# Kernel tuning notes

Hardware: AMD Instinct MI355X
Metric: run time of the kernel (lower is better)

Reference implementation:

```python
import jax, jax.numpy as jnp
import numpy as np

N = 768      # n_proto (number of class prototypes)
D = 128      # trans_feat_num
H = D // 16  # edge-MLP hidden = 8
A = 312      # semantic attribute dim
INIT_TEMP = 0.1
VTEMP = 10.0
STEMP = 10.0
EPS = 1e-8


def _layer_norm(x, g, b, eps=1e-5):
    m = x.mean(-1, keepdims=True)
    v = ((x - m) ** 2).mean(-1, keepdims=True)
    return (x - m) / jnp.sqrt(v + eps) * g + b


def _instance_norm_rows(x, eps=1e-5):
    # torch InstanceNorm1d on 2D input: unbatched (C, L) -> normalize each row, no affine
    m = x.mean(-1, keepdims=True)
    v = ((x - m) ** 2).mean(-1, keepdims=True)
    return (x - m) / jnp.sqrt(v + eps)


def _init_edge(x, temp):
    # pairwise cosine similarity + row softmax
    nrm = jnp.linalg.norm(x, axis=1)
    sim = (x @ x.T) / jnp.maximum(nrm[:, None] * nrm[None, :], EPS)
    return jax.nn.softmax(sim / temp, axis=-1)


def _edge_update(proto, last_edge, W1, b1, W2, b2, temp):
    n, d = proto.shape
    # O(n^2) pairwise squared differences  -> [n*n, d]
    feat = ((proto[:, None, :] - proto[None, :, :]) ** 2).reshape(n * n, d)
    h = jax.nn.relu(_instance_norm_rows(feat @ W1.T + b1))  # [n*n, H]
    e = jnp.tanh(h @ W2.T + b2).reshape(n, n)
    return jax.nn.softmax(e * (last_edge + EPS) / temp, axis=-1)


def _node_update(proto, last_edge, edge, W, b, g, beta):
    extra = last_edge @ proto          # cross-modal message (dist_injection)
    p = edge @ proto                   # same-modal aggregation
    return jax.nn.relu(_layer_norm((p + extra) @ W.T + b, g, beta)) + p


def setup_inputs() -> dict:
    key = jax.random.key(0)
    ks = jax.random.split(key, 9)
    rn = lambda k, shape, s=1.0: jax.random.normal(k, shape, dtype=jnp.float32) * s
    return {
        "visual_proto": rn(ks[0], (N, D)),
        "semantic_proto": rn(ks[1], (N, D)),
        "attribute": rn(ks[2], (N, A)),
        "Wvn": rn(ks[3], (D, D), 0.08), "bvn": jnp.zeros((D,), jnp.float32),
        "gvn": jnp.ones((D,), jnp.float32), "betavn": jnp.zeros((D,), jnp.float32),
        "Wve1": rn(ks[4], (H, D), 0.1), "bve1": jnp.zeros((H,), jnp.float32),
        "Wve2": rn(ks[5], (1, H), 0.3), "bve2": jnp.zeros((1,), jnp.float32),
        "Wsn": rn(ks[6], (D, D), 0.08), "bsn": jnp.zeros((D,), jnp.float32),
        "gsn": jnp.ones((D,), jnp.float32), "betasn": jnp.zeros((D,), jnp.float32),
        "Wse1": rn(ks[7], (H, D), 0.1), "bse1": jnp.zeros((H,), jnp.float32),
        "Wse2": rn(ks[8], (1, H), 0.3), "bse2": jnp.zeros((1,), jnp.float32),
    }


def reference(visual_proto, semantic_proto, attribute,
              Wvn, bvn, gvn, betavn, Wve1, bve1, Wve2, bve2,
              Wsn, bsn, gsn, betasn, Wse1, bse1, Wse2, bse2):
    ve = _init_edge(visual_proto, INIT_TEMP)
    se = _init_edge(attribute, INIT_TEMP)
    vp = _node_update(visual_proto, se, ve, Wvn, bvn, gvn, betavn)
    ve2 = _edge_update(vp, ve, Wve1, bve1, Wve2, bve2, VTEMP)
    sp = _node_update(semantic_proto, ve2, se, Wsn, bsn, gsn, betasn)
    se2 = _edge_update(sp, se, Wse1, bse1, Wse2, bse2, STEMP)
    return vp, sp, ve2, se2
```

## Files before the change

kernel.cpp:

```cpp
#include <hip/hip_runtime.h>
#include <math.h>

#define NN 768
#define DD 128
#define AA 312
#define HH 8
#define CEPS 1e-8f

typedef __attribute__((ext_vector_type(8))) short s8b;
typedef __attribute__((ext_vector_type(4))) float f4v;

__device__ __forceinline__ float wave_sum(float v) {
    #pragma unroll
    for (int o = 32; o; o >>= 1) v += __shfl_down(v, o, 64);
    return v;
}
__device__ __forceinline__ float wave_max(float v) {
    #pragma unroll
    for (int o = 32; o; o >>= 1) v = fmaxf(v, __shfl_down(v, o, 64));
    return v;
}
__device__ __forceinline__ unsigned short f2bf(float f) {
    unsigned u = __float_as_uint(f);
    u += 0x7FFFu + ((u >> 16) & 1u);
    return (unsigned short)(u >> 16);
}

template <int COLS>
__device__ void gram_tile(const float* __restrict__ A, float invtemp, float* __restrict__ sim,
                          int i0, int j0, int tid, float* As, float* Bs) {
    const int tx = tid & 15, ty = tid >> 4;
    const int lr = tid >> 3, lc4 = (tid & 7) * 4;
    float acc00 = 0.f, acc01 = 0.f, acc10 = 0.f, acc11 = 0.f;
    float si0 = 0.f, si1 = 0.f, sj0 = 0.f, sj1 = 0.f;
    for (int kc = 0; kc < COLS; kc += 32) {
        float4 av, bv;
        if (kc + lc4 + 4 <= COLS) {
            av = *(const float4*)(A + (size_t)(i0 + lr) * COLS + kc + lc4);
            bv = *(const float4*)(A + (size_t)(j0 + lr) * COLS + kc + lc4);
        } else {
            float ta[4], tb[4];
            #pragma unroll
            for (int l = 0; l < 4; ++l) {
                int c = kc + lc4 + l;
                ta[l] = (c < COLS) ? A[(size_t)(i0 + lr) * COLS + c] : 0.f;
                tb[l] = (c < COLS) ? A[(size_t)(j0 + lr) * COLS + c] : 0.f;
            }
            av = make_float4(ta[0], ta[1], ta[2], ta[3]);
            bv = make_float4(tb[0], tb[1], tb[2], tb[3]);
        }
        __syncthreads();
        As[(lc4 + 0) * 34 + lr] = av.x; As[(lc4 + 1) * 34 + lr] = av.y;
        As[(lc4 + 2) * 34 + lr] = av.z; As[(lc4 + 3) * 34 + lr] = av.w;
        Bs[(lc4 + 0) * 34 + lr] = bv.x; Bs[(lc4 + 1) * 34 + lr] = bv.y;
        Bs[(lc4 + 2) * 34 + lr] = bv.z; Bs[(lc4 + 3) * 34 + lr] = bv.w;
        __syncthreads();
        #pragma unroll
        for (int k = 0; k < 32; ++k) {
            float2 aa = *(const float2*)&As[k * 34 + 2 * ty];
            float2 bb = *(const float2*)&Bs[k * 34 + 2 * tx];
            acc00 = fmaf(aa.x, bb.x, acc00);
            acc01 = fmaf(aa.x, bb.y, acc01);
            acc10 = fmaf(aa.y, bb.x, acc10);
            acc11 = fmaf(aa.y, bb.y, acc11);
            si0 = fmaf(aa.x, aa.x, si0);
            si1 = fmaf(aa.y, aa.y, si1);
            sj0 = fmaf(bb.x, bb.x, sj0);
            sj1 = fmaf(bb.y, bb.y, sj1);
        }
    }
    const float ni0 = sqrtf(si0), ni1 = sqrtf(si1);
    const float nj0 = sqrtf(sj0), nj1 = sqrtf(sj1);
    float* s0 = sim + (size_t)(i0 + 2 * ty) * NN + j0 + 2 * tx;
    float* s1 = s0 + NN;
    s0[0] = acc00 / fmaxf(ni0 * nj0, CEPS) * invtemp;
    s0[1] = acc01 / fmaxf(ni0 * nj1, CEPS) * invtemp;
    s1[0] = acc10 / fmaxf(ni1 * nj0, CEPS) * invtemp;
    s1[1] = acc11 / fmaxf(ni1 * nj1, CEPS) * invtemp;
}

__global__ __launch_bounds__(256) void gram_prep_kernel(
    const float* __restrict__ visual, const float* __restrict__ attribute,
    const float* __restrict__ Wvn, const float* __restrict__ Wsn, float* __restrict__ simv,
    float* __restrict__ sima, float* __restrict__ WvnT, float* __restrict__ WsnT) {
    __shared__ __align__(16) float smem[2176];
    const int tid = threadIdx.x;
    const int task = blockIdx.x;
    if (task < 576) {
        gram_tile<DD>(visual, 10.f, simv, (task / 24) * 32, (task % 24) * 32, tid, smem,
                      smem + 1088);
    } else if (task < 1152) {
        const int rem = task - 576;
        gram_tile<AA>(attribute, 10.f, sima, (rem / 24) * 32, (rem % 24) * 32, tid, smem,
                      smem + 1088);
    } else {
        const int u = task - 1152;
        const float* S = (u >= 16) ? Wsn : Wvn;
        float* Dt = (u >= 16) ? WsnT : WvnT;
        const int tile = u & 15;
        const int c0 = (tile & 3) * 32, r0 = (tile >> 2) * 32;
        const int tx = tid & 31, ty = tid >> 5;
        #pragma unroll
        for (int rr = ty; rr < 32; rr += 8)
            smem[rr * 33 + tx] = S[(size_t)(r0 + rr) * DD + c0 + tx];
        __syncthreads();
        #pragma unroll
        for (int rr = ty; rr < 32; rr += 8)
            Dt[(size_t)(c0 + rr) * DD + r0 + tx] = smem[tx * 33 + rr];
    }
}

__device__ void softmax_row_g(const float* __restrict__ vr, float* __restrict__ dst, int tid,
                              float* red) {
    float v0 = vr[tid], v1 = vr[tid + 256], v2 = vr[tid + 512];
    float m = wave_max(fmaxf(fmaxf(v0, v1), v2));
    if ((tid & 63) == 0) red[tid >> 6] = m;
    __syncthreads();
    m = fmaxf(fmaxf(red[0], red[1]), fmaxf(red[2], red[3]));
    float e0 = __expf(v0 - m), e1 = __expf(v1 - m), e2 = __expf(v2 - m);
    float sw = wave_sum(e0 + e1 + e2);
    if ((tid & 63) == 0) red[4 + (tid >> 6)] = sw;
    __syncthreads();
    const float s = red[4] + red[5] + red[6] + red[7];
    const float inv = 1.f / s;
    dst[tid] = e0 * inv;
    dst[tid + 256] = e1 * inv;
    dst[tid + 512] = e2 * inv;
}

__global__ __launch_bounds__(256) void softmax_all_kernel(const float* __restrict__ simv,
                                                          const float* __restrict__ sima,
                                                          float* __restrict__ ve,
                                                          float* __restrict__ se) {
    __shared__ float red[8];
    const int task = blockIdx.x;
    const float* src = (task < NN) ? simv + (size_t)task * NN : sima + (size_t)(task - NN) * NN;
    float* dst = (task < NN) ? ve + (size_t)task * NN : se + (size_t)(task - NN) * NN;
    softmax_row_g(src, dst, threadIdx.x, red);
}

__global__ __launch_bounds__(256) void softmax_out_kernel(const float* __restrict__ L,
                                                          float* __restrict__ dst) {
    __shared__ float red[8];
    const int i = blockIdx.x;
    softmax_row_g(L + (size_t)i * NN, dst + (size_t)i * NN, threadIdx.x, red);
}

__device__ void block_softmax768(float* buf, int tid, float* red) {
    const int w = tid >> 6, lane = tid & 63;
    float v0 = buf[tid];
    float v1 = (tid < NN - 512) ? buf[tid + 512] : -3.4e38f;
    float m = wave_max(fmaxf(v0, v1));
    if (lane == 0) red[w] = m;
    __syncthreads();
    m = red[0];
    #pragma unroll
    for (int i = 1; i < 8; ++i) m = fmaxf(m, red[i]);
    float e0 = __expf(v0 - m);
    float e1 = (tid < NN - 512) ? __expf(v1 - m) : 0.f;
    float sw = wave_sum(e0 + e1);
    if (lane == 0) red[8 + w] = sw;
    __syncthreads();
    float s = 0.f;
    #pragma unroll
    for (int i = 0; i < 8; ++i) s += red[8 + i];
    const float inv = 1.f / s;
    buf[tid] = e0 * inv;
    if (tid < NN - 512) buf[tid + 512] = e1 * inv;
    __syncthreads();
}

template <bool EXSM>
__global__ __launch_bounds__(512) void node_kernel(
    const float* __restrict__ P, const float* __restrict__ Ep, const float* __restrict__ ExOrL,
    const float* __restrict__ WT, const float* __restrict__ b, const float* __restrict__ g,
    const float* __restrict__ beta, float* __restrict__ out, const float* __restrict__ W1e,
    short* __restrict__ outb, float* __restrict__ cvec, float* __restrict__ exOut) {
    __shared__ __align__(16) float ep[2][NN], ex[2][NN];
    __shared__ __align__(16) float pp[4][2][DD], xx[4][2][DD];
    __shared__ __align__(16) float qs[2][DD], tps[2][2][DD];
    __shared__ float red[16];
    const int i0 = blockIdx.x * 2;
    const int tid = threadIdx.x;
    const int s = (tid >> 7) & 3, d = tid & 127;
    #pragma unroll
    for (int r = 0; r < 2; ++r)
        for (int k = tid; k < NN; k += 512) {
            ep[r][k] = Ep[(size_t)(i0 + r) * NN + k];
            ex[r][k] = ExOrL[(size_t)(i0 + r) * NN + k];
        }
    __syncthreads();
    if (EXSM) {
        block_softmax768(ex[0], tid, red);
        block_softmax768(ex[1], tid, red);
        #pragma unroll
        for (int r = 0; r < 2; ++r)
            for (int k = tid; k < NN; k += 512) exOut[(size_t)(i0 + r) * NN + k] = ex[r][k];
    }
    float p0 = 0.f, x0 = 0.f, p1 = 0.f, x1 = 0.f;
    const int kb = s * 192;
    #pragma unroll 4
    for (int kk = 0; kk < 192; ++kk) {
        const int k = kb + kk;
        const float pv = P[(size_t)k * DD + d];
        p0 = fmaf(ep[0][k], pv, p0);
        x0 = fmaf(ex[0][k], pv, x0);
        p1 = fmaf(ep[1][k], pv, p1);
        x1 = fmaf(ex[1][k], pv, x1);
    }
    pp[s][0][d] = p0; xx[s][0][d] = x0;
    pp[s][1][d] = p1; xx[s][1][d] = x1;
    __syncthreads();
    const int rr = (tid >> 7) & 1;
    float preg = 0.f;
    if (tid < 256) {
        float p = pp[0][rr][d] + pp[1][rr][d] + pp[2][rr][d] + pp[3][rr][d];
        float x = xx[0][rr][d] + xx[1][rr][d] + xx[2][rr][d] + xx[3][rr][d];
        qs[rr][d] = p + x;
        preg = p;
    }
    __syncthreads();
    {
        const int sc = tid >> 8, rr2 = (tid >> 7) & 1;
        float t = (sc == 0) ? b[d] : 0.f;
        const int c0 = sc * 64;
        #pragma unroll 4
        for (int c = c0; c < c0 + 64; ++c) t = fmaf(qs[rr2][c], WT[(size_t)c * DD + d], t);
        tps[sc][rr2][d] = t;
    }
    __syncthreads();
    float tval = 0.f;
    if (tid < 256) tval = tps[0][rr][d] + tps[1][rr][d];
    float sm = wave_sum(tid < 256 ? tval : 0.f);
    if ((tid & 63) == 0) red[tid >> 6] = sm;
    __syncthreads();
    if (tid < 256) tval -= (red[2 * rr] + red[2 * rr + 1]) * (1.f / DD);
    float s2 = wave_sum(tid < 256 ? tval * tval : 0.f);
    if ((tid & 63) == 0) red[8 + (tid >> 6)] = s2;
    __syncthreads();
    if (tid < 256) {
        const float var = (red[8 + 2 * rr] + red[8 + 2 * rr + 1]) * (1.f / DD);
        const float ln = tval * rsqrtf(var + 1e-5f) * g[d] + beta[d];
        const float val = fmaxf(ln, 0.f) + preg;
        out[(size_t)(i0 + rr) * DD + d] = val;
        outb[(size_t)(i0 + rr) * DD + d] = (short)f2bf(val);
        qs[rr][d] = val;
    }
    __syncthreads();
    if (tid < 16) {
        const int row = tid >> 3, r = tid & 7;
        float ssum = 0.f;
        for (int k = 0; k < DD; ++k) {
            const float pv = qs[row][k];
            ssum = fmaf(W1e[r * DD + k], pv * pv, ssum);
        }
        cvec[(size_t)(i0 + row) * HH + r] = ssum;
    }
}

__global__ __launch_bounds__(256) void edge_gemm_kernel(
    const float* __restrict__ PR, const short* __restrict__ PRb, const float* __restrict__ cvec,
    const float* __restrict__ Elast, const float* __restrict__ W1, const float* __restrict__ b1,
    const float* __restrict__ W2, const float* __restrict__ b2, float invtemp,
    float* __restrict__ Lout) {
    const int bp = blockIdx.x / 3;
    const int i0 = bp * 2;
    const int jbase = (blockIdx.x % 3) * 256;
    const int tid = threadIdx.x;
    const int lane = tid & 63, wave = tid >> 6;
    __shared__ __align__(16) float pi[2][DD];
    __shared__ __align__(16) float w1s[HH * DD];
    __shared__ __align__(16) short a_sw[4 * 64 * 8];
    if (tid < 256) pi[tid >> 7][tid & 127] = PR[(size_t)(i0 + (tid >> 7)) * DD + (tid & 127)];
    ((float4*)w1s)[tid] = ((const float4*)W1)[tid];
    __syncthreads();
    {
        const int t = tid >> 6, m = lane & 15, q = lane >> 4;
        const int il = m >> 3, r = m & 7;
        const int kb = t * 32 + q * 8;
        s8b av;
        #pragma unroll
        for (int e = 0; e < 8; ++e)
            av[e] = (short)f2bf(pi[il][kb + e] * w1s[r * DD + kb + e]);
        *(s8b*)&a_sw[(t * 64 + lane) * 8] = av;
    }
    __syncthreads();
    s8b af[4];
    #pragma unroll
    for (int t = 0; t < 4; ++t) af[t] = *(const s8b*)&a_sw[(t * 64 + lane) * 8];
    const int q = lane >> 4, n = lane & 15;
    const int rbase = (q & 1) * 4;
    const int il = q >> 1;
    const float4 ci4 = *(const float4*)&cvec[(size_t)(i0 + il) * HH + rbase];
    const float4 b14 = *(const float4*)&b1[rbase];
    const float4 w24 = *(const float4*)&W2[rbase];
    const float b2s = b2[0];
    #pragma unroll
    for (int s = 0; s < 4; ++s) {
        const int j = jbase + (wave * 4 + s) * 16 + n;
        f4v acc = {0.f, 0.f, 0.f, 0.f};
        #pragma unroll
        for (int t = 0; t < 4; ++t) {
            const s8b bf = *(const s8b*)(PRb + (size_t)j * DD + t * 32 + q * 8);
            acc = __builtin_amdgcn_mfma_f32_16x16x32_bf16(af[t], bf, acc, 0, 0, 0);
        }
        const float4 cj = *(const float4*)&cvec[(size_t)j * HH + rbase];
        float z[4];
        z[0] = ci4.x + cj.x - 2.f * acc[0] + b14.x;
        z[1] = ci4.y + cj.y - 2.f * acc[1] + b14.y;
        z[2] = ci4.z + cj.z - 2.f * acc[2] + b14.z;
        z[3] = ci4.w + cj.w - 2.f * acc[3] + b14.w;
        float s1 = z[0] + z[1] + z[2] + z[3];
        float s2 = z[0] * z[0] + z[1] * z[1] + z[2] * z[2] + z[3] * z[3];
        s1 += __shfl_xor(s1, 16, 64);
        s2 += __shfl_xor(s2, 16, 64);
        const float mean = s1 * (1.f / HH);
        const float var = fmaxf(s2 * (1.f / HH) - mean * mean, 0.f);
        const float istd = rsqrtf(var + 1e-5f);
        float a2 = 0.f;
        a2 = fmaf(fmaxf((z[0] - mean) * istd, 0.f), w24.x, a2);
        a2 = fmaf(fmaxf((z[1] - mean) * istd, 0.f), w24.y, a2);
        a2 = fmaf(fmaxf((z[2] - mean) * istd, 0.f), w24.z, a2);
        a2 = fmaf(fmaxf((z[3] - mean) * istd, 0.f), w24.w, a2);
        a2 += __shfl_xor(a2, 16, 64);
        const float tv = tanhf(a2 + b2s);
        const float lv = Elast[(size_t)(i0 + il) * NN + j];
        if ((q & 1) == 0) Lout[(size_t)(i0 + il) * NN + j] = tv * (lv + CEPS) * invtemp;
    }
}

extern "C" void kernel_launch(void* const* d_in, const int* in_sizes, int n_in, void* d_out,
                              int out_size, void* d_ws, size_t ws_size, hipStream_t stream) {
    const float* visual    = (const float*)d_in[0];
    const float* semantic  = (const float*)d_in[1];
    const float* attribute = (const float*)d_in[2];
    const float* Wvn  = (const float*)d_in[3];
    const float* bvn  = (const float*)d_in[4];
    const float* gvn  = (const float*)d_in[5];
    const float* betavn = (const float*)d_in[6];
    const float* Wve1 = (const float*)d_in[7];
    const float* bve1 = (const float*)d_in[8];
    const float* Wve2 = (const float*)d_in[9];
    const float* bve2 = (const float*)d_in[10];
    const float* Wsn  = (const float*)d_in[11];
    const float* bsn  = (const float*)d_in[12];
    const float* gsn  = (const float*)d_in[13];
    const float* betasn = (const float*)d_in[14];
    const float* Wse1 = (const float*)d_in[15];
    const float* bse1 = (const float*)d_in[16];
    const float* Wse2 = (const float*)d_in[17];
    const float* bse2 = (const float*)d_in[18];

    float* out = (float*)d_out;
    float* vp  = out;
    float* sp  = out + 98304;
    float* ve2 = out + 196608;
    float* se2 = out + 786432;

    float* ws    = (float*)d_ws;
    float* simv  = ws;
    float* sima  = ws + 589824;
    float* ve    = ws + 1179648;
    float* se    = ws + 1769472;
    float* L     = ws + 2359296;
    float* WvnT  = ws + 2949120;
    float* WsnT  = ws + 2965504;
    float* cvec1 = ws + 2981888;
    float* cvec2 = ws + 2988032;
    short* vpb   = (short*)(ws + 2994176);
    short* spb   = (short*)(ws + 3043328);

    gram_prep_kernel<<<1184, 256, 0, stream>>>(visual, attribute, Wvn, Wsn, simv, sima, WvnT,
                                               WsnT);
    softmax_all_kernel<<<1536, 256, 0, stream>>>(simv, sima, ve, se);
    node_kernel<false><<<NN / 2, 512, 0, stream>>>(visual, ve, se, WvnT, bvn, gvn, betavn, vp,
                                                   Wve1, vpb, cvec1, nullptr);
    edge_gemm_kernel<<<(NN / 2) * 3, 256, 0, stream>>>(vp, vpb, cvec1, ve, Wve1, bve1, Wve2,
                                                       bve2, 0.1f, L);
    node_kernel<true><<<NN / 2, 512, 0, stream>>>(semantic, se, L, WsnT, bsn, gsn, betasn, sp,
                                                  Wse1, spb, cvec2, ve2);
    edge_gemm_kernel<<<(NN / 2) * 3, 256, 0, stream>>>(sp, spb, cvec2, se, Wse1, bse1, Wse2,
                                                       bse2, 0.1f, L);
    softmax_out_kernel<<<NN, 256, 0, stream>>>(L, se2);
}
```

Measured before the change: 196.2 us.

## Fuse init-edge softmax and output softmax into node and edge kernels

The Gram kernel now writes raw dot products plus per-row inverse norms taken from the diagonal tiles. Cosine scaling and the row softmax are recomputed inside the node and edge kernels, so the separate softmax launches and the ve/se/L round trips through global memory go away. The edge kernel now handles full rows, 384 blocks of 512 threads, and applies the final softmax in shared memory before writing the output. In exchange, softmax work is repeated in several kernels, the edge kernel has fewer and larger blocks with more shared memory, and norms now come from the Gram diagonal instead of a separate sum of squares.

After: 203.5 us. 3.7% more time.

```diff
diff --git a/kernel.cpp b/kernel.cpp
--- a/kernel.cpp
+++ b/kernel.cpp
@@ -26,13 +26,37 @@
     return (unsigned short)(u >> 16);
 }
 
+__device__ void block_softmax768(float* buf, int tid, float* red) {
+    const int w = tid >> 6, lane = tid & 63;
+    float v0 = buf[tid];
+    float v1 = (tid < NN - 512) ? buf[tid + 512] : -3.4e38f;
+    float m = wave_max(fmaxf(v0, v1));
+    if (lane == 0) red[w] = m;
+    __syncthreads();
+    m = red[0];
+    #pragma unroll
+    for (int i = 1; i < 8; ++i) m = fmaxf(m, red[i]);
+    float e0 = __expf(v0 - m);
+    float e1 = (tid < NN - 512) ? __expf(v1 - m) : 0.f;
+    float sw = wave_sum(e0 + e1);
+    if (lane == 0) red[8 + w] = sw;
+    __syncthreads();
+    float s = 0.f;
+    #pragma unroll
+    for (int i = 0; i < 8; ++i) s += red[8 + i];
+    const float inv = 1.f / s;
+    buf[tid] = e0 * inv;
+    if (tid < NN - 512) buf[tid + 512] = e1 * inv;
+    __syncthreads();
+}
+
 template <int COLS>
-__device__ void gram_tile(const float* __restrict__ A, float invtemp, float* __restrict__ sim,
-                          int i0, int j0, int tid, float* As, float* Bs) {
+__device__ void gram_tile_raw(const float* __restrict__ A, float* __restrict__ sim,
+                              float* __restrict__ invn, int i0, int j0, int tid, float* As,
+                              float* Bs) {
     const int tx = tid & 15, ty = tid >> 4;
     const int lr = tid >> 3, lc4 = (tid & 7) * 4;
     float acc00 = 0.f, acc01 = 0.f, acc10 = 0.f, acc11 = 0.f;
-    float si0 = 0.f, si1 = 0.f, sj0 = 0.f, sj1 = 0.f;
     for (int kc = 0; kc < COLS; kc += 32) {
         float4 av, bv;
         if (kc + lc4 + 4 <= COLS) {
@@ -63,36 +87,33 @@
             acc01 = fmaf(aa.x, bb.y, acc01);
             acc10 = fmaf(aa.y, bb.x, acc10);
             acc11 = fmaf(aa.y, bb.y, acc11);
-            si0 = fmaf(aa.x, aa.x, si0);
-            si1 = fmaf(aa.y, aa.y, si1);
-            sj0 = fmaf(bb.x, bb.x, sj0);
-            sj1 = fmaf(bb.y, bb.y, sj1);
-        }
-    }
-    const float ni0 = sqrtf(si0), ni1 = sqrtf(si1);
-    const float nj0 = sqrtf(sj0), nj1 = sqrtf(sj1);
+        }
+    }
     float* s0 = sim + (size_t)(i0 + 2 * ty) * NN + j0 + 2 * tx;
     float* s1 = s0 + NN;
-    s0[0] = acc00 / fmaxf(ni0 * nj0, CEPS) * invtemp;
-    s0[1] = acc01 / fmaxf(ni0 * nj1, CEPS) * invtemp;
-    s1[0] = acc10 / fmaxf(ni1 * nj0, CEPS) * invtemp;
-    s1[1] = acc11 / fmaxf(ni1 * nj1, CEPS) * invtemp;
+    s0[0] = acc00; s0[1] = acc01;
+    s1[0] = acc10; s1[1] = acc11;
+    if (i0 == j0 && tx == ty) {
+        invn[i0 + 2 * tx] = 1.f / sqrtf(fmaxf(acc00, 1e-24f));
+        invn[i0 + 2 * tx + 1] = 1.f / sqrtf(fmaxf(acc11, 1e-24f));
+    }
 }
 
 __global__ __launch_bounds__(256) void gram_prep_kernel(
     const float* __restrict__ visual, const float* __restrict__ attribute,
     const float* __restrict__ Wvn, const float* __restrict__ Wsn, float* __restrict__ simv,
-    float* __restrict__ sima, float* __restrict__ WvnT, float* __restrict__ WsnT) {
+    float* __restrict__ sima, float* __restrict__ WvnT, float* __restrict__ WsnT,
+    float* __restrict__ invnv, float* __restrict__ invna) {
     __shared__ __align__(16) float smem[2176];
     const int tid = threadIdx.x;
     const int task = blockIdx.x;
     if (task < 576) {
-        gram_tile<DD>(visual, 10.f, simv, (task / 24) * 32, (task % 24) * 32, tid, smem,
-                      smem + 1088);
+        gram_tile_raw<DD>(visual, simv, invnv, (task / 24) * 32, (task % 24) * 32, tid, smem,
+                          smem + 1088);
     } else if (task < 1152) {
         const int rem = task - 576;
-        gram_tile<AA>(attribute, 10.f, sima, (rem / 24) * 32, (rem % 24) * 32, tid, smem,
-                      smem + 1088);
+        gram_tile_raw<AA>(attribute, sima, invna, (rem / 24) * 32, (rem % 24) * 32, tid, smem,
+                          smem + 1088);
     } else {
         const int u = task - 1152;
         const float* S = (u >= 16) ? Wsn : Wvn;
@@ -110,72 +131,13 @@
     }
 }
 
-__device__ void softmax_row_g(const float* __restrict__ vr, float* __restrict__ dst, int tid,
-                              float* red) {
-    float v0 = vr[tid], v1 = vr[tid + 256], v2 = vr[tid + 512];
-    float m = wave_max(fmaxf(fmaxf(v0, v1), v2));
-    if ((tid & 63) == 0) red[tid >> 6] = m;
-    __syncthreads();
-    m = fmaxf(fmaxf(red[0], red[1]), fmaxf(red[2], red[3]));
-    float e0 = __expf(v0 - m), e1 = __expf(v1 - m), e2 = __expf(v2 - m);
-    float sw = wave_sum(e0 + e1 + e2);
-    if ((tid & 63) == 0) red[4 + (tid >> 6)] = sw;
-    __syncthreads();
-    const float s = red[4] + red[5] + red[6] + red[7];
-    const float inv = 1.f / s;
-    dst[tid] = e0 * inv;
-    dst[tid + 256] = e1 * inv;
-    dst[tid + 512] = e2 * inv;
-}
-
-__global__ __launch_bounds__(256) void softmax_all_kernel(const float* __restrict__ simv,
-                                                          const float* __restrict__ sima,
-                                                          float* __restrict__ ve,
-                                                          float* __restrict__ se) {
-    __shared__ float red[8];
-    const int task = blockIdx.x;
-    const float* src = (task < NN) ? simv + (size_t)task * NN : sima + (size_t)(task - NN) * NN;
-    float* dst = (task < NN) ? ve + (size_t)task * NN : se + (size_t)(task - NN) * NN;
-    softmax_row_g(src, dst, threadIdx.x, red);
-}
-
-__global__ __launch_bounds__(256) void softmax_out_kernel(const float* __restrict__ L,
-                                                          float* __restrict__ dst) {
-    __shared__ float red[8];
-    const int i = blockIdx.x;
-    softmax_row_g(L + (size_t)i * NN, dst + (size_t)i * NN, threadIdx.x, red);
-}
-
-__device__ void block_softmax768(float* buf, int tid, float* red) {
-    const int w = tid >> 6, lane = tid & 63;
-    float v0 = buf[tid];
-    float v1 = (tid < NN - 512) ? buf[tid + 512] : -3.4e38f;
-    float m = wave_max(fmaxf(v0, v1));
-    if (lane == 0) red[w] = m;
-    __syncthreads();
-    m = red[0];
-    #pragma unroll
-    for (int i = 1; i < 8; ++i) m = fmaxf(m, red[i]);
-    float e0 = __expf(v0 - m);
-    float e1 = (tid < NN - 512) ? __expf(v1 - m) : 0.f;
-    float sw = wave_sum(e0 + e1);
-    if (lane == 0) red[8 + w] = sw;
-    __syncthreads();
-    float s = 0.f;
-    #pragma unroll
-    for (int i = 0; i < 8; ++i) s += red[8 + i];
-    const float inv = 1.f / s;
-    buf[tid] = e0 * inv;
-    if (tid < NN - 512) buf[tid + 512] = e1 * inv;
-    __syncthreads();
-}
-
 template <bool EXSM>
 __global__ __launch_bounds__(512) void node_kernel(
-    const float* __restrict__ P, const float* __restrict__ Ep, const float* __restrict__ ExOrL,
-    const float* __restrict__ WT, const float* __restrict__ b, const float* __restrict__ g,
-    const float* __restrict__ beta, float* __restrict__ out, const float* __restrict__ W1e,
-    short* __restrict__ outb, float* __restrict__ cvec, float* __restrict__ exOut) {
+    const float* __restrict__ P, const float* __restrict__ EpRaw,
+    const float* __restrict__ invnP, const float* __restrict__ Ex,
+    const float* __restrict__ invnX, const float* __restrict__ WT, const float* __restrict__ b,
+    const float* __restrict__ g, const float* __restrict__ beta, float* __restrict__ out,
+    const float* __restrict__ W1e, short* __restrict__ outb, float* __restrict__ cvec) {
     __shared__ __align__(16) float ep[2][NN], ex[2][NN];
     __shared__ __align__(16) float pp[4][2][DD], xx[4][2][DD];
     __shared__ __align__(16) float qs[2][DD], tps[2][2][DD];
@@ -183,19 +145,23 @@
     const int i0 = blockIdx.x * 2;
     const int tid = threadIdx.x;
     const int s = (tid >> 7) & 3, d = tid & 127;
+    const float cp0 = 10.f * invnP[i0], cp1 = 10.f * invnP[i0 + 1];
+    const float cx0 = EXSM ? 10.f * invnX[i0] : 0.f;
+    const float cx1 = EXSM ? 10.f * invnX[i0 + 1] : 0.f;
     #pragma unroll
     for (int r = 0; r < 2; ++r)
         for (int k = tid; k < NN; k += 512) {
-            ep[r][k] = Ep[(size_t)(i0 + r) * NN + k];
-            ex[r][k] = ExOrL[(size_t)(i0 + r) * NN + k];
-        }
-    __syncthreads();
+            ep[r][k] = EpRaw[(size_t)(i0 + r) * NN + k] * (r ? cp1 : cp0) * invnP[k];
+            float x = Ex[(size_t)(i0 + r) * NN + k];
+            if (EXSM) x *= (r ? cx1 : cx0) * invnX[k];
+            ex[r][k] = x;
+        }
+    __syncthreads();
+    block_softmax768(ep[0], tid, red);
+    block_softmax768(ep[1], tid, red);
     if (EXSM) {
         block_softmax768(ex[0], tid, red);
         block_softmax768(ex[1], tid, red);
-        #pragma unroll
-        for (int r = 0; r < 2; ++r)
-            for (int k = tid; k < NN; k += 512) exOut[(size_t)(i0 + r) * NN + k] = ex[r][k];
     }
     float p0 = 0.f, x0 = 0.f, p1 = 0.f, x1 = 0.f;
     const int kb = s * 192;
@@ -258,23 +224,31 @@
     }
 }
 
-__global__ __launch_bounds__(256) void edge_gemm_kernel(
+__global__ __launch_bounds__(512) void edge_full_kernel(
     const float* __restrict__ PR, const short* __restrict__ PRb, const float* __restrict__ cvec,
-    const float* __restrict__ Elast, const float* __restrict__ W1, const float* __restrict__ b1,
-    const float* __restrict__ W2, const float* __restrict__ b2, float invtemp,
-    float* __restrict__ Lout) {
-    const int bp = blockIdx.x / 3;
-    const int i0 = bp * 2;
-    const int jbase = (blockIdx.x % 3) * 256;
+    const float* __restrict__ lastRaw, const float* __restrict__ invnL,
+    const float* __restrict__ W1, const float* __restrict__ b1, const float* __restrict__ W2,
+    const float* __restrict__ b2, float invtemp, float* __restrict__ Eout) {
+    const int i0 = blockIdx.x * 2;
     const int tid = threadIdx.x;
     const int lane = tid & 63, wave = tid >> 6;
     __shared__ __align__(16) float pi[2][DD];
     __shared__ __align__(16) float w1s[HH * DD];
     __shared__ __align__(16) short a_sw[4 * 64 * 8];
+    __shared__ __align__(16) float lrow[2][NN];
+    __shared__ __align__(16) float logits[2][NN];
+    __shared__ float red[16];
     if (tid < 256) pi[tid >> 7][tid & 127] = PR[(size_t)(i0 + (tid >> 7)) * DD + (tid & 127)];
-    ((float4*)w1s)[tid] = ((const float4*)W1)[tid];
-    __syncthreads();
-    {
+    else ((float4*)w1s)[tid - 256] = ((const float4*)W1)[tid - 256];
+    const float cl0 = 10.f * invnL[i0], cl1 = 10.f * invnL[i0 + 1];
+    #pragma unroll
+    for (int r = 0; r < 2; ++r)
+        for (int k = tid; k < NN; k += 512)
+            lrow[r][k] = lastRaw[(size_t)(i0 + r) * NN + k] * (r ? cl1 : cl0) * invnL[k];
+    __syncthreads();
+    block_softmax768(lrow[0], tid, red);
+    block_softmax768(lrow[1], tid, red);
+    if (tid < 256) {
         const int t = tid >> 6, m = lane & 15, q = lane >> 4;
         const int il = m >> 3, r = m & 7;
         const int kb = t * 32 + q * 8;
@@ -296,8 +270,8 @@
     const float4 w24 = *(const float4*)&W2[rbase];
     const float b2s = b2[0];
     #pragma unroll
-    for (int s = 0; s < 4; ++s) {
-        const int j = jbase + (wave * 4 + s) * 16 + n;
+    for (int s = 0; s < 6; ++s) {
+        const int j = (wave * 6 + s) * 16 + n;
         f4v acc = {0.f, 0.f, 0.f, 0.f};
         #pragma unroll
         for (int t = 0; t < 4; ++t) {
@@ -324,9 +298,15 @@
         a2 = fmaf(fmaxf((z[3] - mean) * istd, 0.f), w24.w, a2);
         a2 += __shfl_xor(a2, 16, 64);
         const float tv = tanhf(a2 + b2s);
-        const float lv = Elast[(size_t)(i0 + il) * NN + j];
-        if ((q & 1) == 0) Lout[(size_t)(i0 + il) * NN + j] = tv * (lv + CEPS) * invtemp;
-    }
+        if ((q & 1) == 0) logits[il][j] = tv * (lrow[il][j] + CEPS) * invtemp;
+    }
+    __syncthreads();
+    block_softmax768(logits[0], tid, red);
+    block_softmax768(logits[1], tid, red);
+    #pragma unroll
+    for (int r = 0; r < 2; ++r)
+        for (int k = tid; k < NN; k += 512)
+            Eout[(size_t)(i0 + r) * NN + k] = logits[r][k];
 }
 
 extern "C" void kernel_launch(void* const* d_in, const int* in_sizes, int n_in, void* d_out,
@@ -360,26 +340,23 @@
     float* ws    = (float*)d_ws;
     float* simv  = ws;
     float* sima  = ws + 589824;
-    float* ve    = ws + 1179648;
-    float* se    = ws + 1769472;
-    float* L     = ws + 2359296;
-    float* WvnT  = ws + 2949120;
-    float* WsnT  = ws + 2965504;
-    float* cvec1 = ws + 2981888;
-    float* cvec2 = ws + 2988032;
-    short* vpb   = (short*)(ws + 2994176);
-    short* spb   = (short*)(ws + 3043328);
+    float* WvnT  = ws + 1179648;
+    float* WsnT  = ws + 1196032;
+    float* invnv = ws + 1212416;
+    float* invna = ws + 1213184;
+    float* cvec1 = ws + 1213952;
+    float* cvec2 = ws + 1220096;
+    short* vpb   = (short*)(ws + 1226240);
+    short* spb   = (short*)(ws + 1275392);
 
     gram_prep_kernel<<<1184, 256, 0, stream>>>(visual, attribute, Wvn, Wsn, simv, sima, WvnT,
-                                               WsnT);
-    softmax_all_kernel<<<1536, 256, 0, stream>>>(simv, sima, ve, se);
-    node_kernel<false><<<NN / 2, 512, 0, stream>>>(visual, ve, se, WvnT, bvn, gvn, betavn, vp,
-                                                   Wve1, vpb, cvec1, nullptr);
-    edge_gemm_kernel<<<(NN / 2) * 3, 256, 0, stream>>>(vp, vpb, cvec1, ve, Wve1, bve1, Wve2,
-                                                       bve2, 0.1f, L);
-    node_kernel<true><<<NN / 2, 512, 0, stream>>>(semantic, se, L, WsnT, bsn, gsn, betasn, sp,
-                                                  Wse1, spb, cvec2, ve2);
-    edge_gemm_kernel<<<(NN / 2) * 3, 256, 0, stream>>>(sp, spb, cvec2, se, Wse1, bse1, Wse2,
-                                                       bse2, 0.1f, L);
-    softmax_out_kernel<<<NN, 256, 0, stream>>>(L, se2);
-}
+                                               WsnT, invnv, invna);
+    node_kernel<true><<<NN / 2, 512, 0, stream>>>(visual, simv, invnv, sima, invna, WvnT, bvn,
+                                                  gvn, betavn, vp, Wve1, vpb, cvec1);
+    edge_full_kernel<<<NN / 2, 512, 0, stream>>>(vp, vpb, cvec1, simv, invnv, Wve1, bve1, Wve2,
+                                                 bve2, 0.1f, ve2);
+    node_kernel<false><<<NN / 2, 512, 0, stream>>>(semantic, sima, invna, ve2, nullptr, WsnT,
+                                                   bsn, gsn, betasn, sp, Wse1, spb, cvec2);
+    edge_full_kernel<<<NN / 2, 512, 0, stream>>>(sp, spb, cvec2, sima, invna, Wse1, bse1, Wse2,
+                                                 bse2, 0.1f, se2);
+}
```
